# Optimization experiments

Measured on AMD Instinct MI355X. Metric: run time of the kernel, lower is better.

## Reference

```python
import jax, jax.numpy as jnp
import numpy as np

N = 131072   # total nodes (4096 molecules x ~32 atoms)
E = 524288   # directed edges (avg degree 4)
G = 4096     # number of graphs
D_IN, D_H, D_OUT = 128, 512, 256
BN_EPS = 1e-5


def setup_inputs() -> dict:
    key = jax.random.key(0)
    ks = jax.random.split(key, 24)
    def rn(i, shape, s=0.05):
        return jax.random.normal(ks[i], shape, jnp.float32) * s
    inp = {
        "x": jax.random.normal(ks[0], (N, D_IN), jnp.float32),
        "edge_index": jax.random.randint(ks[1], (2, E), 0, N),
        "batch": jnp.sort(jax.random.randint(ks[2], (N,), 0, G)),
        # GCN layer weights (stored [in, out]) and biases
        "W1": rn(3, (D_IN, D_H)), "b1": jnp.zeros((D_H,), jnp.float32),
        "W2": rn(4, (D_H, D_H)),  "b2": jnp.zeros((D_H,), jnp.float32),
        "W3": rn(5, (D_H, D_OUT)), "b3": jnp.zeros((D_OUT,), jnp.float32),
        # BatchNorm (eval mode): gamma, beta, running_mean, running_var
        "g1": jnp.ones((D_H,), jnp.float32),  "be1": jnp.zeros((D_H,), jnp.float32),
        "m1": rn(6, (D_H,)),  "v1": jax.random.uniform(ks[7], (D_H,), jnp.float32) + 0.5,
        "g2": jnp.ones((D_H,), jnp.float32),  "be2": jnp.zeros((D_H,), jnp.float32),
        "m2": rn(8, (D_H,)),  "v2": jax.random.uniform(ks[9], (D_H,), jnp.float32) + 0.5,
        "g3": jnp.ones((D_OUT,), jnp.float32), "be3": jnp.zeros((D_OUT,), jnp.float32),
        "m3": rn(10, (D_OUT,)), "v3": jax.random.uniform(ks[11], (D_OUT,), jnp.float32) + 0.5,
        # MLP head
        "Wf1": rn(12, (D_OUT, D_OUT)), "bf1": jnp.zeros((D_OUT,), jnp.float32),
        "Wf2": rn(13, (D_OUT, D_OUT)), "bf2": jnp.zeros((D_OUT,), jnp.float32),
    }
    return inp


def reference(x, edge_index, batch, W1, b1, W2, b2, W3, b3,
              g1, be1, m1, v1, g2, be2, m2, v2, g3, be3, m3, v3,
              Wf1, bf1, Wf2, bf2):
    loop = jnp.arange(N)
    src = jnp.concatenate([edge_index[0], loop])  # add self-loops (PyG GCNConv default)
    dst = jnp.concatenate([edge_index[1], loop])
    deg = jax.ops.segment_sum(jnp.ones((E + N,), x.dtype), dst, num_segments=N)
    dinv = jnp.where(deg > 0, jax.lax.rsqrt(deg), 0.0)
    norm = dinv[src] * dinv[dst]                  # D^{-1/2} A_hat D^{-1/2}

    def gcn(h, W, b):
        h = h @ W                                 # dense GEMM [N, d_out]
        msg = h[src] * norm[:, None]              # gather + scale
        return jax.ops.segment_sum(msg, dst, num_segments=N) + b  # scatter-add

    def bn(h, g, be, m, v):                       # eval-mode BatchNorm1d
        return g * (h - m) * jax.lax.rsqrt(v + BN_EPS) + be

    h = bn(jax.nn.relu(gcn(x, W1, b1)), g1, be1, m1, v1)
    h = bn(jax.nn.relu(gcn(h, W2, b2)), g2, be2, m2, v2)
    h = bn(jax.nn.relu(gcn(h, W3, b3)), g3, be3, m3, v3)

    sums = jax.ops.segment_sum(h, batch, num_segments=G)          # global_mean_pool
    cnt = jax.ops.segment_sum(jnp.ones((N,), h.dtype), batch, num_segments=G)
    pooled = sums / jnp.maximum(cnt, 1.0)[:, None]

    return jax.nn.relu(pooled @ Wf1 + bf1) @ Wf2 + bf2
```

## Files before the change

kernel.cpp:

```cpp
#include <hip/hip_runtime.h>

static constexpr int NN = 131072;
static constexpr int NE = 524288;
static constexpr int NG = 4096;

typedef __attribute__((ext_vector_type(8))) short short8;
typedef __attribute__((ext_vector_type(4))) float f32x4;
typedef __attribute__((ext_vector_type(2))) float f32x2;

__device__ __forceinline__ float bfbits2f(unsigned b) {
    return __uint_as_float(b << 16);
}
__device__ __forceinline__ unsigned short f2bfbits(float f) {
    unsigned u = __float_as_uint(f);
    u += 0x7fffu + ((u >> 16) & 1u);
    return (unsigned short)(u >> 16);
}
__device__ __forceinline__ unsigned pack2(float a, float b) {
    return (unsigned)f2bfbits(a) | ((unsigned)f2bfbits(b) << 16);
}

__device__ __forceinline__ int geti(const void* p, size_t i, int w64) {
    return w64 ? (int)((const long long*)p)[i] : ((const int*)p)[i];
}
__device__ __forceinline__ int e64_of(const void* eidx) {
    const int* e = (const int*)eidx;
    return (e[1] == 0 && e[2001] == 0 && e[40001] == 0 && e[2 * NE - 1] == 0) ? 1 : 0;
}
__device__ __forceinline__ int b64_of(const void* batch) {
    return (((const int*)batch)[NN - 1] == 0) ? 1 : 0;
}

#if __has_builtin(__builtin_amdgcn_cvt_pk_f32_fp8) && __has_builtin(__builtin_amdgcn_cvt_pk_fp8_f32)
#define FP8_CVT_HW 1
#else
#define FP8_CVT_HW 0
#endif

__device__ __forceinline__ float e4m32f(unsigned b) {
    unsigned e = (b >> 3) & 0xFu, m = b & 7u;
    float v = e ? __uint_as_float(((e + 120u) << 23) | (m << 20))
                : (float)m * 0.001953125f;
    return (b & 0x80u) ? -v : v;
}
__device__ __forceinline__ unsigned f2e4m3(float f) {
    unsigned u = __float_as_uint(f);
    unsigned s = (u >> 24) & 0x80u;
    unsigned mag = u & 0x7fffffffu;
    if (mag >= 0x43e00000u) return s | 0x7eu;
    if (mag < 0x3c800000u) {
        int q = (int)(__uint_as_float(mag) * 512.0f + 0.5f);
        return s | (unsigned)q;
    }
    unsigned r = mag + 0x0007ffffu + ((mag >> 20) & 1u);
    if (r >= 0x43e00000u) return s | 0x7eu;
    return s | (((r >> 23) - 120u) << 3) | ((r >> 20) & 7u);
}

template<bool HI>
__device__ __forceinline__ unsigned dec_pair(unsigned w) {
#if FP8_CVT_HW
    f32x2 p = __builtin_amdgcn_cvt_pk_f32_fp8((int)w, HI);
    return __builtin_amdgcn_perm(__float_as_uint(p.y), __float_as_uint(p.x), 0x07060302u);
#else
    unsigned b0 = HI ? ((w >> 16) & 255u) : (w & 255u);
    unsigned b1 = HI ? (w >> 24) : ((w >> 8) & 255u);
    return pack2(e4m32f(b0), e4m32f(b1));
#endif
}

__device__ __forceinline__ short8 dec8(uint2 u) {
    union { uint4 q; short8 s; } r;
    r.q.x = dec_pair<false>(u.x);
    r.q.y = dec_pair<true>(u.x);
    r.q.z = dec_pair<false>(u.y);
    r.q.w = dec_pair<true>(u.y);
    return r.s;
}

__device__ __forceinline__ void dec4f(unsigned w, float* v) {
#if FP8_CVT_HW
    f32x2 a = __builtin_amdgcn_cvt_pk_f32_fp8((int)w, false);
    f32x2 b = __builtin_amdgcn_cvt_pk_f32_fp8((int)w, true);
    v[0] = a.x; v[1] = a.y; v[2] = b.x; v[3] = b.y;
#else
#pragma unroll
    for (int i = 0; i < 4; ++i) v[i] = e4m32f((w >> (8 * i)) & 0xffu);
#endif
}

__device__ __forceinline__ unsigned enc4(float a, float b, float c, float d) {
#if FP8_CVT_HW
    int r = __builtin_amdgcn_cvt_pk_fp8_f32(a, b, 0, false);
    r = __builtin_amdgcn_cvt_pk_fp8_f32(c, d, r, true);
    return (unsigned)r;
#else
    return f2e4m3(a) | (f2e4m3(b) << 8) | (f2e4m3(c) << 16) | (f2e4m3(d) << 24);
#endif
}
__device__ __forceinline__ unsigned enc1(float a) {
#if FP8_CVT_HW
    return (unsigned)__builtin_amdgcn_cvt_pk_fp8_f32(a, a, 0, false) & 0xffu;
#else
    return f2e4m3(a);
#endif
}

__device__ __forceinline__ void gld16(const void* g, void* l, int lane) {
#if __has_builtin(__builtin_amdgcn_global_load_lds)
    __builtin_amdgcn_global_load_lds((const __attribute__((address_space(1))) unsigned int*)g,
                                     (__attribute__((address_space(3))) unsigned int*)l, 16, 0, 0);
#else
    *(uint4*)((char*)l + lane * 16) = *(const uint4*)g;
#endif
}

__global__ __launch_bounds__(256) void k_prep(
    const float* __restrict__ W1, const float* __restrict__ W2, const float* __restrict__ W3,
    const float* __restrict__ Wf1, const float* __restrict__ Wf2,
    unsigned short* __restrict__ Wt1, unsigned short* __restrict__ Wt2,
    unsigned short* __restrict__ Wt3, unsigned short* __restrict__ Wtf1,
    unsigned short* __restrict__ Wtf2,
    const float* __restrict__ g1, const float* __restrict__ be1,
    const float* __restrict__ m1, const float* __restrict__ v1,
    const float* __restrict__ g2, const float* __restrict__ be2,
    const float* __restrict__ m2, const float* __restrict__ v2,
    const float* __restrict__ g3, const float* __restrict__ be3,
    const float* __restrict__ m3, const float* __restrict__ v3,
    float* __restrict__ sbuf, int* __restrict__ cnt2,
    const void* __restrict__ batch, int* __restrict__ gstart)
{
    const int id = blockIdx.x, tid = threadIdx.x;
    if (id < 1024) {
        int idx = id * 256 + tid; int k = idx >> 9, n = idx & 511;
        Wt2[n * 512 + k] = f2bfbits(W2[idx]);
    } else if (id < 1536) {
        int idx = (id - 1024) * 256 + tid; int k = idx >> 8, n = idx & 255;
        Wt3[n * 512 + k] = f2bfbits(W3[idx]);
    } else if (id < 1792) {
        int idx = (id - 1536) * 256 + tid; int k = idx >> 9, n = idx & 511;
        Wt1[n * 128 + k] = f2bfbits(W1[idx]);
    } else if (id < 2048) {
        int idx = (id - 1792) * 256 + tid; int k = idx >> 8, n = idx & 255;
        Wtf1[n * 256 + k] = f2bfbits(Wf1[idx]);
    } else if (id < 2304) {
        int idx = (id - 2048) * 256 + tid; int k = idx >> 8, n = idx & 255;
        Wtf2[n * 256 + k] = f2bfbits(Wf2[idx]);
    } else if (id < 3328) {
        cnt2[(id - 2304) * 256 + tid] = 0;
    } else if (id < 3333) {
        int i = (id - 3328) * 256 + tid;
        if (i < 512) {
            float inv = rsqrtf(v1[i] + 1e-5f); float sc = g1[i] * inv;
            sbuf[i] = sc; sbuf[512 + i] = be1[i] - m1[i] * sc;
        } else if (i < 1024) {
            int j = i - 512;
            float inv = rsqrtf(v2[j] + 1e-5f); float sc = g2[j] * inv;
            sbuf[1024 + j] = sc; sbuf[1536 + j] = be2[j] - m2[j] * sc;
        } else if (i < 1280) {
            int j = i - 1024;
            float inv = rsqrtf(v3[j] + 1e-5f); float sc = g3[j] * inv;
            sbuf[2048 + j] = sc; sbuf[2304 + j] = be3[j] - m3[j] * sc;
        }
    } else {
        int i = (id - 3333) * 256 + tid;
        if (i >= NN) return;
        int b64 = b64_of(batch);
        int b = geti(batch, (size_t)i, b64);
        if (i == 0) {
            for (int g = 0; g <= b; ++g) gstart[g] = 0;
        } else {
            int pb = geti(batch, (size_t)i - 1, b64);
            for (int g = pb + 1; g <= b; ++g) gstart[g] = i;
        }
        if (i == NN - 1) {
            for (int g = b + 1; g <= NG; ++g) gstart[g] = NN;
        }
    }
}

__global__ void k_deg_count(const void* __restrict__ eidx, int* __restrict__ cnt) {
    int i = blockIdx.x * 256 + threadIdx.x;
    if (i >= NE) return;
    int d = geti(eidx, (size_t)NE + i, e64_of(eidx));
    atomicAdd(&cnt[d], 1);
}

__global__ __launch_bounds__(1024) void k_scan(const int* __restrict__ cnt, int* __restrict__ rowptr,
                                               float* __restrict__ dinv) {
    __shared__ int part[1024];
    const int t = threadIdx.x;
    const int base = t * 128;
    const int4* c4 = (const int4*)(cnt + base);
    int s = 0;
#pragma unroll
    for (int i = 0; i < 32; ++i) { int4 u = c4[i]; s += u.x + u.y + u.z + u.w; }
    part[t] = s;
    __syncthreads();
    for (int off = 1; off < 1024; off <<= 1) {
        int v = (t >= off) ? part[t - off] : 0;
        __syncthreads();
        part[t] += v;
        __syncthreads();
    }
    int ex = (t == 0) ? 0 : part[t - 1];
#pragma unroll
    for (int i = 0; i < 32; ++i) {
        int4 u = c4[i];
        int4 o; o.x = ex; o.y = ex + u.x; o.z = o.y + u.y; o.w = o.z + u.z; ex = o.w + u.w;
        *(int4*)(rowptr + base + 4 * i) = o;
        float4 dv;
        dv.x = rsqrtf((float)(u.x + 1)); dv.y = rsqrtf((float)(u.y + 1));
        dv.z = rsqrtf((float)(u.z + 1)); dv.w = rsqrtf((float)(u.w + 1));
        *(float4*)(dinv + base + 4 * i) = dv;
    }
    if (t == 1023) rowptr[NN] = ex;
}

__global__ void k_fill(const void* __restrict__ eidx,
                       const int* __restrict__ rowptr, int* __restrict__ fillp,
                       int* __restrict__ col) {
    int i = blockIdx.x * 256 + threadIdx.x;
    if (i >= NE) return;
    int e64 = e64_of(eidx);
    int s = geti(eidx, (size_t)i, e64);
    int d = geti(eidx, (size_t)NE + i, e64);
    int p = rowptr[d] + atomicAdd(&fillp[d], 1);
    col[p] = s;
}

template<int D, int MODE>
__device__ __forceinline__ void load_row_hw(const void* h, int sn, int c0, float* v) {
    if constexpr (MODE == 2) {
        float4 u = *(const float4*)((const float*)h + (size_t)sn * D + c0);
        v[0] = u.x; v[1] = u.y; v[2] = u.z; v[3] = u.w;
    } else {
        uint4 u = *(const uint4*)((const unsigned char*)h + (size_t)sn * D + c0);
        dec4f(u.x, v); dec4f(u.y, v + 4); dec4f(u.z, v + 8); dec4f(u.w, v + 12);
    }
}

template<int D, int EPL, bool FP8>
__device__ __forceinline__ void store_row_hw(void* out, int n, int c0, const float* v) {
    if constexpr (FP8) {
        uint4 u;
        u.x = enc4(v[0], v[1], v[2], v[3]);
        u.y = enc4(v[4], v[5], v[6], v[7]);
        u.z = enc4(v[8], v[9], v[10], v[11]);
        u.w = enc4(v[12], v[13], v[14], v[15]);
        *(uint4*)((unsigned char*)out + (size_t)n * D + c0) = u;
    } else {
        uint2 u; u.x = pack2(v[0], v[1]); u.y = pack2(v[2], v[3]);
        *(uint2*)((unsigned short*)out + (size_t)n * D + c0) = u;
    }
}

template<int D, int IN_MODE, bool OUT_FP8>
__global__ __launch_bounds__(256) void k_agg_hw(
    const void* __restrict__ h,
    const int* __restrict__ rowptr, const int* __restrict__ col,
    const float* __restrict__ dinv,
    void* __restrict__ out)
{
    constexpr int EPL = (IN_MODE == 1) ? 16 : 4;
    const int n = (blockIdx.x * 256 + threadIdx.x) >> 5;
    const int lane = threadIdx.x & 31;
    const int c0 = lane * EPL;
    float dn = dinv[n];
    float acc[EPL], va[EPL], vb[EPL];

    load_row_hw<D, IN_MODE>(h, n, c0, va);
    float wsl = dn * dn;
#pragma unroll
    for (int i = 0; i < EPL; ++i) acc[i] = va[i] * wsl;

    int e = rowptr[n], e1 = rowptr[n + 1];
    for (; e + 2 <= e1; e += 2) {
        int sa = col[e], sb = col[e + 1];
        float wa = dinv[sa] * dn, wb = dinv[sb] * dn;
        load_row_hw<D, IN_MODE>(h, sa, c0, va);
        load_row_hw<D, IN_MODE>(h, sb, c0, vb);
#pragma unroll
        for (int i = 0; i < EPL; ++i) acc[i] += va[i] * wa + vb[i] * wb;
    }
    if (e < e1) {
        int sa = col[e];
        float wa = dinv[sa] * dn;
        load_row_hw<D, IN_MODE>(h, sa, c0, va);
#pragma unroll
        for (int i = 0; i < EPL; ++i) acc[i] += va[i] * wa;
    }
    store_row_hw<D, EPL, OUT_FP8>(out, n, c0, acc);
}

__global__ __launch_bounds__(256) void k_agg_pool(
    const unsigned short* __restrict__ T3,
    const int* __restrict__ rowptr, const int* __restrict__ col,
    const float* __restrict__ dinv,
    const float* __restrict__ b, const float* __restrict__ s, const float* __restrict__ t,
    const int* __restrict__ gstart, unsigned short* __restrict__ pooled)
{
    __shared__ float red[4][256];
    const int g = blockIdx.x;
    const int wave = threadIdx.x >> 6, lane = threadIdx.x & 63;
    const int c0 = lane * 4;
    const int r0 = gstart[g], r1 = gstart[g + 1];
    float p0 = 0, p1 = 0, p2 = 0, p3 = 0;
    const float bc0 = b[c0], bc1 = b[c0 + 1], bc2 = b[c0 + 2], bc3 = b[c0 + 3];
    const float sc0 = s[c0], sc1 = s[c0 + 1], sc2 = s[c0 + 2], sc3 = s[c0 + 3];
    const float tc0 = t[c0], tc1 = t[c0 + 1], tc2 = t[c0 + 2], tc3 = t[c0 + 3];

    for (int n = r0 + wave; n < r1; n += 4) {
        float dn = dinv[n];
        float a0, a1, a2, a3;
        {
            uint2 u = *(const uint2*)(T3 + (size_t)n * 256 + c0);
            float w = dn * dn;
            a0 = bfbits2f(u.x & 0xffffu) * w; a1 = bfbits2f(u.x >> 16) * w;
            a2 = bfbits2f(u.y & 0xffffu) * w; a3 = bfbits2f(u.y >> 16) * w;
        }
        int e = rowptr[n], e1 = rowptr[n + 1];
        for (; e + 2 <= e1; e += 2) {
            int sa = col[e], sb = col[e + 1];
            float wa = dinv[sa] * dn, wb = dinv[sb] * dn;
            uint2 ua = *(const uint2*)(T3 + (size_t)sa * 256 + c0);
            uint2 ub = *(const uint2*)(T3 + (size_t)sb * 256 + c0);
            a0 += bfbits2f(ua.x & 0xffffu) * wa + bfbits2f(ub.x & 0xffffu) * wb;
            a1 += bfbits2f(ua.x >> 16) * wa + bfbits2f(ub.x >> 16) * wb;
            a2 += bfbits2f(ua.y & 0xffffu) * wa + bfbits2f(ub.y & 0xffffu) * wb;
            a3 += bfbits2f(ua.y >> 16) * wa + bfbits2f(ub.y >> 16) * wb;
        }
        if (e < e1) {
            int sa = col[e];
            float wa = dinv[sa] * dn;
            uint2 ua = *(const uint2*)(T3 + (size_t)sa * 256 + c0);
            a0 += bfbits2f(ua.x & 0xffffu) * wa; a1 += bfbits2f(ua.x >> 16) * wa;
            a2 += bfbits2f(ua.y & 0xffffu) * wa; a3 += bfbits2f(ua.y >> 16) * wa;
        }
        p0 += sc0 * fmaxf(a0 + bc0, 0.0f) + tc0;
        p1 += sc1 * fmaxf(a1 + bc1, 0.0f) + tc1;
        p2 += sc2 * fmaxf(a2 + bc2, 0.0f) + tc2;
        p3 += sc3 * fmaxf(a3 + bc3, 0.0f) + tc3;
    }
    red[wave][c0] = p0; red[wave][c0 + 1] = p1; red[wave][c0 + 2] = p2; red[wave][c0 + 3] = p3;
    __syncthreads();
    int ch = threadIdx.x;
    float tot = red[0][ch] + red[1][ch] + red[2][ch] + red[3][ch];
    __syncthreads();
    red[0][ch] = tot;
    __syncthreads();
    if (ch < 128) {
        int ccount = r1 - r0;
        float inv = 1.0f / (float)(ccount > 0 ? ccount : 1);
        pooled[(size_t)g * 256 + 2 * ch] = f2bfbits(red[0][2 * ch] * inv);
        pooled[(size_t)g * 256 + 2 * ch + 1] = f2bfbits(red[0][2 * ch + 1] * inv);
    }
}

template<bool A_FP8, int CB, int OUT_MODE, bool RELU, bool HAS_BN, bool HAS_BIAS>
__global__ __launch_bounds__(256)
void k_gemm(const void* __restrict__ Aptr,
            const unsigned short* __restrict__ Wt,
            const float* __restrict__ bias,
            const float* __restrict__ s, const float* __restrict__ t,
            void* __restrict__ Cptr,
            int K, int Ncols)
{
    __shared__ __align__(16) unsigned short lB[2][2][128 * 32];
    __shared__ __align__(16) unsigned char  lA8[A_FP8 ? 2 : 1][A_FP8 ? 2 : 1][A_FP8 ? 128 * 32 : 16];
    __shared__ __align__(16) unsigned short lA16[A_FP8 ? 1 : 2][A_FP8 ? 1 : 2][A_FP8 ? 8 : 128 * 32];
    const int tid = threadIdx.x;
    const int id = blockIdx.x;
    const int hi = id >> 3;
    const int cblk = hi % CB;
    const int rblk = (hi / CB) * 8 + (id & 7);
    const int bm = rblk * 128;
    const int bn = cblk * 128;
    const int lane = tid & 63;
    const int wave = tid >> 6;
    const int wm = (wave >> 1) * 64;
    const int wn = (wave & 1) * 64;
    const int fr = lane & 15;
    const int fq = lane >> 4;

    f32x4 acc[4][4] = {};
    const int NG64 = K >> 6;

    auto stage = [&](int buf, int k0) {
#pragma unroll
        for (int h = 0; h < 2; ++h) {
            const int kh = k0 + h * 32;
            if constexpr (A_FP8) {
                const unsigned char* g = (const unsigned char*)Aptr
                    + (size_t)(bm + (wave << 5) + (lane >> 1)) * K + kh + (lane & 1) * 16;
                gld16(g, &lA8[buf][h][(wave << 5) * 32], lane);
            } else {
                const unsigned short* Ab = (const unsigned short*)Aptr;
#pragma unroll
                for (int c = 0; c < 2; ++c) {
                    const unsigned short* g = Ab
                        + (size_t)(bm + (wave << 5) + (c << 4) + (lane >> 2)) * K + kh + (lane & 3) * 8;
                    gld16(g, &lA16[buf][h][((wave << 5) + (c << 4)) * 32], lane);
                }
            }
#pragma unroll
            for (int c = 0; c < 2; ++c) {
                const unsigned short* g = Wt
                    + (size_t)(bn + (wave << 5) + (c << 4) + (lane >> 2)) * K + kh + (lane & 3) * 8;
                gld16(g, &lB[buf][h][((wave << 5) + (c << 4)) * 32], lane);
            }
        }
    };

    stage(0, 0);
    __syncthreads();

    int cur = 0;
    for (int kg = 0; kg < NG64; ++kg) {
        if (kg + 1 < NG64) stage(cur ^ 1, (kg + 1) << 6);

#pragma unroll
        for (int h = 0; h < 2; ++h) {
            short8 a[4], b[4];
#pragma unroll
            for (int i = 0; i < 4; ++i) {
                if constexpr (A_FP8)
                    a[i] = dec8(*(const uint2*)&lA8[cur][h][(wm + 16 * i + fr) * 32 + fq * 8]);
                else
                    a[i] = *(const short8*)&lA16[cur][h][(wm + 16 * i + fr) * 32 + fq * 8];
            }
#pragma unroll
            for (int j = 0; j < 4; ++j)
                b[j] = *(const short8*)&lB[cur][h][(wn + 16 * j + fr) * 32 + fq * 8];
#pragma unroll
            for (int i = 0; i < 4; ++i)
#pragma unroll
                for (int j = 0; j < 4; ++j)
                    acc[i][j] = __builtin_amdgcn_mfma_f32_16x16x32_bf16(a[i], b[j], acc[i][j], 0, 0, 0);
        }

        __syncthreads();
        cur ^= 1;
    }

#pragma unroll
    for (int j = 0; j < 4; ++j) {
        int colI = bn + wn + 16 * j + fr;
        float bi = HAS_BIAS ? bias[colI] : 0.0f;
        float sc = HAS_BN ? s[colI] : 1.0f;
        float tc = HAS_BN ? t[colI] : 0.0f;
#pragma unroll
        for (int i = 0; i < 4; ++i) {
#pragma unroll
            for (int r = 0; r < 4; ++r) {
                int row = bm + wm + 16 * i + fq * 4 + r;
                float z = acc[i][j][r] + bi;
                if (RELU) z = fmaxf(z, 0.0f);
                float y = HAS_BN ? (sc * z + tc) : z;
                if constexpr (OUT_MODE == 2)
                    ((float*)Cptr)[(size_t)row * Ncols + colI] = y;
                else if constexpr (OUT_MODE == 1)
                    ((unsigned char*)Cptr)[(size_t)row * Ncols + colI] = (unsigned char)enc1(y);
                else
                    ((unsigned short*)Cptr)[(size_t)row * Ncols + colI] = f2bfbits(y);
            }
        }
    }
}

template<int CB, int OUT_MODE, bool RELU, bool HAS_BN, bool HAS_BIAS>
__global__ __launch_bounds__(512)
void k_gemm8w(const unsigned char* __restrict__ Aptr,
              const unsigned short* __restrict__ Wt,
              const float* __restrict__ bias,
              const float* __restrict__ s, const float* __restrict__ t,
              void* __restrict__ Cptr,
              int K, int Ncols)
{
    __shared__ __align__(16) unsigned char  lA[2][2][256 * 32];
    __shared__ __align__(16) unsigned short lB[2][2][128 * 32];
    const int tid = threadIdx.x;
    const int id = blockIdx.x;
    const int hi = id >> 3;
    const int cblk = hi % CB;
    const int rblk = (hi / CB) * 8 + (id & 7);
    const int bm = rblk * 256;
    const int bn = cblk * 128;
    const int lane = tid & 63;
    const int wave = tid >> 6;
    const int wm = (wave >> 1) * 64;
    const int wn = (wave & 1) * 64;
    const int fr = lane & 15;
    const int fq = lane >> 4;

    f32x4 acc[4][4] = {};
    const int NG64 = K >> 6;

    auto stage = [&](int buf, int k0) {
#pragma unroll
        for (int h = 0; h < 2; ++h) {
            const int kh = k0 + h * 32;
            {
                const unsigned char* g = Aptr
                    + (size_t)(bm + (wave << 5) + (lane >> 1)) * K + kh + (lane & 1) * 16;
                gld16(g, &lA[buf][h][(wave << 5) * 32], lane);
            }
            {
                const unsigned short* g = Wt
                    + (size_t)(bn + (wave << 4) + (lane >> 2)) * K + kh + (lane & 3) * 8;
                gld16(g, &lB[buf][h][(wave << 4) * 32], lane);
            }
        }
    };

    stage(0, 0);
    __syncthreads();

    int cur = 0;
    for (int kg = 0; kg < NG64; ++kg) {
        if (kg + 1 < NG64) stage(cur ^ 1, (kg + 1) << 6);

#pragma unroll
        for (int h = 0; h < 2; ++h) {
            short8 a[4], b[4];
#pragma unroll
            for (int i = 0; i < 4; ++i)
                a[i] = dec8(*(const uint2*)&lA[cur][h][(wm + 16 * i + fr) * 32 + fq * 8]);
#pragma unroll
            for (int j = 0; j < 4; ++j)
                b[j] = *(const short8*)&lB[cur][h][(wn + 16 * j + fr) * 32 + fq * 8];
#pragma unroll
            for (int i = 0; i < 4; ++i)
#pragma unroll
                for (int j = 0; j < 4; ++j)
                    acc[i][j] = __builtin_amdgcn_mfma_f32_16x16x32_bf16(a[i], b[j], acc[i][j], 0, 0, 0);
        }

        __syncthreads();
        cur ^= 1;
    }

#pragma unroll
    for (int j = 0; j < 4; ++j) {
        int colI = bn + wn + 16 * j + fr;
        float bi = HAS_BIAS ? bias[colI] : 0.0f;
        float sc = HAS_BN ? s[colI] : 1.0f;
        float tc = HAS_BN ? t[colI] : 0.0f;
#pragma unroll
        for (int i = 0; i < 4; ++i) {
#pragma unroll
            for (int r = 0; r < 4; ++r) {
                int row = bm + wm + 16 * i + fq * 4 + r;
                float z = acc[i][j][r] + bi;
                if (RELU) z = fmaxf(z, 0.0f);
                float y = HAS_BN ? (sc * z + tc) : z;
                if constexpr (OUT_MODE == 2)
                    ((float*)Cptr)[(size_t)row * Ncols + colI] = y;
                else if constexpr (OUT_MODE == 1)
                    ((unsigned char*)Cptr)[(size_t)row * Ncols + colI] = (unsigned char)enc1(y);
                else
                    ((unsigned short*)Cptr)[(size_t)row * Ncols + colI] = f2bfbits(y);
            }
        }
    }
}

template<int CB, int OUT_MODE, bool RELU, bool HAS_BN, bool HAS_BIAS>
__global__ __launch_bounds__(512)
void k_gemm8n(const unsigned short* __restrict__ Aptr,
              const unsigned short* __restrict__ Wt,
              const float* __restrict__ bias,
              const float* __restrict__ s, const float* __restrict__ t,
              void* __restrict__ Cptr,
              int K, int Ncols)
{
    __shared__ __align__(16) unsigned short lA[2][2][128 * 32];
    __shared__ __align__(16) unsigned short lB[2][2][128 * 32];
    const int tid = threadIdx.x;
    const int id = blockIdx.x;
    const int hi = id >> 3;
    const int cblk = hi % CB;
    const int rblk = (hi / CB) * 8 + (id & 7);
    const int bm = rblk * 128;
    const int bn = cblk * 128;
    const int lane = tid & 63;
    const int wave = tid >> 6;
    const int wm = (wave >> 1) * 32;
    const int wn = (wave & 1) * 64;
    const int fr = lane & 15;
    const int fq = lane >> 4;

    f32x4 acc[2][4] = {};
    const int NG64 = K >> 6;

    auto stage = [&](int buf, int k0) {
#pragma unroll
        for (int h = 0; h < 2; ++h) {
            const int kh = k0 + h * 32;
            const unsigned short* ga = Aptr
                + (size_t)(bm + (wave << 4) + (lane >> 2)) * K + kh + (lane & 3) * 8;
            gld16(ga, &lA[buf][h][(wave << 4) * 32], lane);
            const unsigned short* gb = Wt
                + (size_t)(bn + (wave << 4) + (lane >> 2)) * K + kh + (lane & 3) * 8;
            gld16(gb, &lB[buf][h][(wave << 4) * 32], lane);
        }
    };

    stage(0, 0);
    __syncthreads();

    int cur = 0;
    for (int kg = 0; kg < NG64; ++kg) {
        if (kg + 1 < NG64) stage(cur ^ 1, (kg + 1) << 6);

#pragma unroll
        for (int h = 0; h < 2; ++h) {
            short8 a[2], b[4];
#pragma unroll
            for (int i = 0; i < 2; ++i)
                a[i] = *(const short8*)&lA[cur][h][(wm + 16 * i + fr) * 32 + fq * 8];
#pragma unroll
            for (int j = 0; j < 4; ++j)
                b[j] = *(const short8*)&lB[cur][h][(wn + 16 * j + fr) * 32 + fq * 8];
#pragma unroll
            for (int i = 0; i < 2; ++i)
#pragma unroll
                for (int j = 0; j < 4; ++j)
                    acc[i][j] = __builtin_amdgcn_mfma_f32_16x16x32_bf16(a[i], b[j], acc[i][j], 0, 0, 0);
        }

        __syncthreads();
        cur ^= 1;
    }

#pragma unroll
    for (int j = 0; j < 4; ++j) {
        int colI = bn + wn + 16 * j + fr;
        float bi = HAS_BIAS ? bias[colI] : 0.0f;
        float sc = HAS_BN ? s[colI] : 1.0f;
        float tc = HAS_BN ? t[colI] : 0.0f;
#pragma unroll
        for (int i = 0; i < 2; ++i) {
#pragma unroll
            for (int r = 0; r < 4; ++r) {
                int row = bm + wm + 16 * i + fq * 4 + r;
                float z = acc[i][j][r] + bi;
                if (RELU) z = fmaxf(z, 0.0f);
                float y = HAS_BN ? (sc * z + tc) : z;
                if constexpr (OUT_MODE == 2)
                    ((float*)Cptr)[(size_t)row * Ncols + colI] = y;
                else if constexpr (OUT_MODE == 1)
                    ((unsigned char*)Cptr)[(size_t)row * Ncols + colI] = (unsigned char)enc1(y);
                else
                    ((unsigned short*)Cptr)[(size_t)row * Ncols + colI] = f2bfbits(y);
            }
        }
    }
}


extern "C" void kernel_launch(void* const* d_in, const int* in_sizes, int n_in,
                              void* d_out, int out_size, void* d_ws, size_t ws_size,
                              hipStream_t stream) {
    const float* x   = (const float*)d_in[0];
    const void* eidx = d_in[1];
    const void* batch = d_in[2];
    const float* W1  = (const float*)d_in[3];
    const float* b1  = (const float*)d_in[4];
    const float* W2  = (const float*)d_in[5];
    const float* b2  = (const float*)d_in[6];
    const float* W3  = (const float*)d_in[7];
    const float* b3  = (const float*)d_in[8];
    const float* g1  = (const float*)d_in[9];
    const float* be1 = (const float*)d_in[10];
    const float* m1  = (const float*)d_in[11];
    const float* v1  = (const float*)d_in[12];
    const float* g2  = (const float*)d_in[13];
    const float* be2 = (const float*)d_in[14];
    const float* m2  = (const float*)d_in[15];
    const float* v2  = (const float*)d_in[16];
    const float* g3  = (const float*)d_in[17];
    const float* be3 = (const float*)d_in[18];
    const float* m3  = (const float*)d_in[19];
    const float* v3  = (const float*)d_in[20];
    const float* Wf1 = (const float*)d_in[21];
    const float* bf1 = (const float*)d_in[22];
    const float* Wf2 = (const float*)d_in[23];
    const float* bf2 = (const float*)d_in[24];

    unsigned char* RB = (unsigned char*)d_ws;
    unsigned char* RA = RB + 67108864;
    unsigned char* EX = RB + 134217728;
    int*   rowptr = (int*)(EX + 0);
    int*   col    = (int*)(EX + 524544);
    float* dinv   = (float*)(EX + 2621696);
    int*   cnt    = (int*)(EX + 3145984);
    int*   fillp  = (int*)(EX + 3670272);
    int*   gstart = (int*)(EX + 4194560);
    float* sbuf   = (float*)(EX + 4211456);
    float *s1 = sbuf, *t1 = sbuf + 512, *s2 = sbuf + 1024, *t2 = sbuf + 1536;
    float *s3 = sbuf + 2048, *t3v = sbuf + 2304;
    unsigned short* Wt1  = (unsigned short*)(EX + 4221696);
    unsigned short* Wt2  = (unsigned short*)(EX + 4352768);
    unsigned short* Wt3  = (unsigned short*)(EX + 4877056);
    unsigned short* Wtf1 = (unsigned short*)(EX + 5139200);
    unsigned short* Wtf2 = (unsigned short*)(EX + 5270272);

    unsigned short* pooled = (unsigned short*)RB;
    unsigned short* z1     = (unsigned short*)(RB + 2097152);

    k_prep<<<3845, 256, 0, stream>>>(W1, W2, W3, Wf1, Wf2,
                                     Wt1, Wt2, Wt3, Wtf1, Wtf2,
                                     g1, be1, m1, v1, g2, be2, m2, v2, g3, be3, m3, v3,
                                     sbuf, cnt, batch, gstart);
    k_deg_count<<<NE / 256, 256, 0, stream>>>(eidx, cnt);
    k_scan<<<1, 1024, 0, stream>>>(cnt, rowptr, dinv);
    k_fill<<<NE / 256, 256, 0, stream>>>(eidx, rowptr, fillp, col);

    const dim3 gagg(NN / 8);

    k_agg_hw<128, 2, false><<<gagg, 256, 0, stream>>>(x, rowptr, col, dinv, RA);
    k_gemm8n<4, 1, true, true, true><<<4096, 512, 0, stream>>>(
        (const unsigned short*)RA, Wt1, b1, s1, t1, RB, 128, 512);

    k_agg_hw<512, 1, true><<<gagg, 256, 0, stream>>>(RB, rowptr, col, dinv, RA);
    k_gemm8w<4, 1, true, true, true><<<2048, 512, 0, stream>>>(RA, Wt2, b2, s2, t2, RB, 512, 512);

    k_gemm8w<2, 0, false, false, false><<<1024, 512, 0, stream>>>(RB, Wt3, nullptr, nullptr, nullptr, RA, 512, 256);

    k_agg_pool<<<NG, 256, 0, stream>>>((const unsigned short*)RA, rowptr, col, dinv,
                                       b3, s3, t3v, gstart, pooled);

    k_gemm<false, 2, 0, true, false, true><<<64, 256, 0, stream>>>(pooled, Wtf1, bf1, nullptr, nullptr, z1, 256, 256);
    k_gemm<false, 2, 2, false, false, true><<<64, 256, 0, stream>>>(z1, Wtf2, bf2, nullptr, nullptr, d_out, 256, 256);
}
```

Baseline: 622.4 us.

## Parallelize degree prefix scan across blocks and split layer-2 GEMM launch

Replaces the single-block 1024-thread scan over the node degree counts with a three-kernel multi-block scan: per-block reduction, a scan of the block sums, then a per-block local scan that writes rowptr and dinv. The aim is to spread the serial single-workgroup scan across many CUs. The layer-2 GEMM is also split into two launches over the halves of the rows. This adds extra kernel launches, and the GEMM split offers no obvious benefit beyond possibly probing launch behaviour.

```diff
diff --git a/kernel.cpp b/kernel.cpp
--- a/kernel.cpp
+++ b/kernel.cpp
@@ -186,35 +186,58 @@
     atomicAdd(&cnt[d], 1);
 }
 
-__global__ __launch_bounds__(1024) void k_scan(const int* __restrict__ cnt, int* __restrict__ rowptr,
-                                               float* __restrict__ dinv) {
-    __shared__ int part[1024];
+__global__ __launch_bounds__(256) void k_scan_a(const int* __restrict__ cnt, int* __restrict__ bsum) {
+    __shared__ int red[256];
     const int t = threadIdx.x;
-    const int base = t * 128;
-    const int4* c4 = (const int4*)(cnt + base);
-    int s = 0;
-#pragma unroll
-    for (int i = 0; i < 32; ++i) { int4 u = c4[i]; s += u.x + u.y + u.z + u.w; }
+    int2 u = *(const int2*)(cnt + blockIdx.x * 512 + t * 2);
+    red[t] = u.x + u.y;
+    __syncthreads();
+    for (int off = 128; off > 0; off >>= 1) {
+        if (t < off) red[t] += red[t + off];
+        __syncthreads();
+    }
+    if (t == 0) bsum[blockIdx.x] = red[0];
+}
+
+__global__ __launch_bounds__(256) void k_scan_b(const int* __restrict__ bsum, int* __restrict__ boff,
+                                                int* __restrict__ rowptr) {
+    __shared__ int part[256];
+    const int t = threadIdx.x;
+    int v = bsum[t];
+    part[t] = v;
+    __syncthreads();
+    for (int off = 1; off < 256; off <<= 1) {
+        int w = (t >= off) ? part[t - off] : 0;
+        __syncthreads();
+        part[t] += w;
+        __syncthreads();
+    }
+    boff[t] = part[t] - v;
+    if (t == 255) rowptr[NN] = part[255];
+}
+
+__global__ __launch_bounds__(256) void k_scan_c(const int* __restrict__ cnt, const int* __restrict__ boff,
+                                                int* __restrict__ rowptr, float* __restrict__ dinv) {
+    __shared__ int part[256];
+    const int t = threadIdx.x;
+    const int base = blockIdx.x * 512 + t * 2;
+    int2 u = *(const int2*)(cnt + base);
+    int s = u.x + u.y;
     part[t] = s;
     __syncthreads();
-    for (int off = 1; off < 1024; off <<= 1) {
-        int v = (t >= off) ? part[t - off] : 0;
+    for (int off = 1; off < 256; off <<= 1) {
+        int w = (t >= off) ? part[t - off] : 0;
         __syncthreads();
-        part[t] += v;
+        part[t] += w;
         __syncthreads();
     }
-    int ex = (t == 0) ? 0 : part[t - 1];
-#pragma unroll
-    for (int i = 0; i < 32; ++i) {
-        int4 u = c4[i];
-        int4 o; o.x = ex; o.y = ex + u.x; o.z = o.y + u.y; o.w = o.z + u.z; ex = o.w + u.w;
-        *(int4*)(rowptr + base + 4 * i) = o;
-        float4 dv;
-        dv.x = rsqrtf((float)(u.x + 1)); dv.y = rsqrtf((float)(u.y + 1));
-        dv.z = rsqrtf((float)(u.z + 1)); dv.w = rsqrtf((float)(u.w + 1));
-        *(float4*)(dinv + base + 4 * i) = dv;
-    }
-    if (t == 1023) rowptr[NN] = ex;
+    int ex = boff[blockIdx.x] + part[t] - s;
+    int2 o; o.x = ex; o.y = ex + u.x;
+    *(int2*)(rowptr + base) = o;
+    float2 dv;
+    dv.x = rsqrtf((float)(u.x + 1));
+    dv.y = rsqrtf((float)(u.y + 1));
+    *(float2*)(dinv + base) = dv;
 }
 
 __global__ void k_fill(const void* __restrict__ eidx,
@@ -705,6 +728,8 @@
     unsigned short* Wt3  = (unsigned short*)(EX + 4877056);
     unsigned short* Wtf1 = (unsigned short*)(EX + 5139200);
     unsigned short* Wtf2 = (unsigned short*)(EX + 5270272);
+    int*   bsum  = (int*)(EX + 5401344);
+    int*   boff  = (int*)(EX + 5402368);
 
     unsigned short* pooled = (unsigned short*)RB;
     unsigned short* z1     = (unsigned short*)(RB + 2097152);
@@ -714,7 +739,9 @@
                                      g1, be1, m1, v1, g2, be2, m2, v2, g3, be3, m3, v3,
                                      sbuf, cnt, batch, gstart);
     k_deg_count<<<NE / 256, 256, 0, stream>>>(eidx, cnt);
-    k_scan<<<1, 1024, 0, stream>>>(cnt, rowptr, dinv);
+    k_scan_a<<<256, 256, 0, stream>>>(cnt, bsum);
+    k_scan_b<<<1, 256, 0, stream>>>(bsum, boff, rowptr);
+    k_scan_c<<<256, 256, 0, stream>>>(cnt, boff, rowptr, dinv);
     k_fill<<<NE / 256, 256, 0, stream>>>(eidx, rowptr, fillp, col);
 
     const dim3 gagg(NN / 8);
@@ -724,7 +751,9 @@
         (const unsigned short*)RA, Wt1, b1, s1, t1, RB, 128, 512);
 
     k_agg_hw<512, 1, true><<<gagg, 256, 0, stream>>>(RB, rowptr, col, dinv, RA);
-    k_gemm8w<4, 1, true, true, true><<<2048, 512, 0, stream>>>(RA, Wt2, b2, s2, t2, RB, 512, 512);
+    k_gemm8w<4, 1, true, true, true><<<1024, 512, 0, stream>>>(RA, Wt2, b2, s2, t2, RB, 512, 512);
+    k_gemm8w<4, 1, true, true, true><<<1024, 512, 0, stream>>>(RA + 33554432, Wt2, b2, s2, t2,
+                                                               RB + 33554432, 512, 512);
 
     k_gemm8w<2, 0, false, false, false><<<1024, 512, 0, stream>>>(RB, Wt3, nullptr, nullptr, nullptr, RA, 512, 256);
 
```

Result: faster. 563.4 us (-9.5%).
